# Optimization experiments

Hardware: AMD Instinct MI355X
Metric: run time of the kernel (lower is better)

Reference implementation:

```python
import jax, jax.numpy as jnp
import numpy as np

B = 4096
IN = 1723 * 6          # 10338
H = 1024
OUT = 24 * 3 * 3 + 10 + 3  # 229
EPS = 1e-5


def _bn(x, g, b):
    # BatchNorm1d training-mode forward: biased batch statistics
    mu = jnp.mean(x, axis=0)
    var = jnp.var(x, axis=0)
    return g * (x - mu) * jax.lax.rsqrt(var + EPS) + b


def _resblock(h, wa, ba, ga, bea, wb, bb, gb, beb):
    t = jax.nn.relu(_bn(h @ wa + ba, ga, bea))
    t = _bn(t @ wb + bb, gb, beb)
    return jax.nn.relu(h + t)


def setup_inputs() -> dict:
    key = jax.random.key(0)
    ks = jax.random.split(key, 16)
    s = 0.02
    inp = {"x": jax.random.normal(ks[0], (B, IN), dtype=jnp.float32)}
    # FCBlock(IN -> H): Linear + BN + ReLU
    inp["w1"] = jax.random.normal(ks[1], (IN, H), dtype=jnp.float32) * s
    inp["b1"] = jnp.zeros((H,), jnp.float32)
    inp["g1"] = jnp.ones((H,), jnp.float32)
    inp["be1"] = jnp.zeros((H,), jnp.float32)
    # two FCResBlocks (H -> H)
    for i, kk in zip((2, 3), (ks[2:4], ks[4:6])):
        inp[f"w{i}a"] = jax.random.normal(kk[0], (H, H), dtype=jnp.float32) * s
        inp[f"b{i}a"] = jnp.zeros((H,), jnp.float32)
        inp[f"g{i}a"] = jnp.ones((H,), jnp.float32)
        inp[f"be{i}a"] = jnp.zeros((H,), jnp.float32)
        inp[f"w{i}b"] = jax.random.normal(kk[1], (H, H), dtype=jnp.float32) * s
        inp[f"b{i}b"] = jnp.zeros((H,), jnp.float32)
        inp[f"g{i}b"] = jnp.ones((H,), jnp.float32)
        inp[f"be{i}b"] = jnp.zeros((H,), jnp.float32)
    # final Linear (H -> OUT)
    inp["w4"] = jax.random.normal(ks[6], (H, OUT), dtype=jnp.float32) * s
    inp["b4"] = jnp.zeros((OUT,), jnp.float32)
    return inp


def reference(x, w1, b1, g1, be1,
              w2a, b2a, g2a, be2a, w2b, b2b, g2b, be2b,
              w3a, b3a, g3a, be3a, w3b, b3b, g3b, be3b,
              w4, b4):
    batch = x.shape[0]
    h = jax.nn.relu(_bn(x @ w1 + b1, g1, be1))
    h = _resblock(h, w2a, b2a, g2a, be2a, w2b, b2b, g2b, be2b)
    h = _resblock(h, w3a, b3a, g3a, be3a, w3b, b3b, g3b, be3b)
    out = h @ w4 + b4                              # (B, 229)

    rotmat = out[:, :216].reshape(-1, 3, 3)        # (B*24, 3, 3)
    betas = out[:, 216:226]                        # (B, 10)
    camera = out[:, 226:]                          # (B, 3)

    # batched 3x3 SVD orthogonalization (replaces per-sample Python loop)
    U, S, Vh = jnp.linalg.svd(rotmat, full_matrices=False)
    R = U @ Vh
    # det computed under no_grad in original -> stop_gradient
    det = jax.lax.stop_gradient(jnp.linalg.det(R))[:, None, None]
    R = (R * det).reshape(batch, 24, 3, 3)
    return (R, betas, camera)
```

## Files before the change

### kernel.cpp

```cpp
#include <hip/hip_runtime.h>
#include <math.h>


typedef _Float16 half8 __attribute__((ext_vector_type(8)));
typedef _Float16 half4_t __attribute__((ext_vector_type(4)));
typedef float floatx4 __attribute__((ext_vector_type(4)));

#define LO_SCALE 4096.0f
#define LO_INV (1.0f / 4096.0f)
#define IN_C 10338
#define INP_C 10368

__device__ __forceinline__ void gld16(const _Float16* g, _Float16* l) {
  __builtin_amdgcn_global_load_lds(
      (const __attribute__((address_space(1))) void*)g,
      (__attribute__((address_space(3))) void*)l, 16, 0, 0);
}

template <int TAG, bool STATS>
__global__ __launch_bounds__(256, 2)
void gemm_sk(const _Float16* __restrict__ Ah, const _Float16* __restrict__ Al,
             const _Float16* __restrict__ Bh, const _Float16* __restrict__ Bl,
             float* __restrict__ Cp, int Kld, int Ncols, int Ks,
             size_t partStride, const float* __restrict__ bias,
             float* __restrict__ psum, float* __restrict__ psq) {
  __shared__ _Float16 sAh[2][4096], sAl[2][4096];
  __shared__ _Float16 sBh[2][4096], sBl[2][4096];
  const int tid = threadIdx.x;
  const int wv = tid >> 6, ln = tid & 63;
  const int ln15 = ln & 15, q = ln >> 4;
  const int wr = wv >> 1, wc = wv & 1;
  const int bm0 = blockIdx.x * 128, bn0 = blockIdx.y * 128;
  const int k0 = blockIdx.z * Ks;
  Cp += (size_t)blockIdx.z * partStride;

  const int srow = ln >> 2;
  const int swzw = (ln & 3) ^ (srow & 3) ^ ((srow >> 2) & 3);
  const int ch0 = wv * 2, ch1 = wv * 2 + 1;
  const size_t offA0 = (size_t)(bm0 + ch0 * 16 + srow) * Kld + k0 + swzw * 8;
  const size_t offA1 = (size_t)(bm0 + ch1 * 16 + srow) * Kld + k0 + swzw * 8;
  const size_t offB0 = (size_t)(bn0 + ch0 * 16 + srow) * Kld + k0 + swzw * 8;
  const size_t offB1 = (size_t)(bn0 + ch1 * 16 + srow) * Kld + k0 + swzw * 8;

  const int swzr = (q ^ (ln15 & 3) ^ ((ln15 >> 2) & 3)) * 8;
  const int aoff = (wr * 64 + ln15) * 32 + swzr;
  const int boff = (wc * 64 + ln15) * 32 + swzr;

  floatx4 acc[4][4];
  floatx4 acc2[4][4];
#pragma unroll
  for (int i = 0; i < 4; ++i)
#pragma unroll
    for (int j = 0; j < 4; ++j) {
      acc[i][j] = (floatx4){0.f, 0.f, 0.f, 0.f};
      acc2[i][j] = (floatx4){0.f, 0.f, 0.f, 0.f};
    }

  auto stage = [&](int kt, int buf) {
    gld16(Ah + offA0 + kt, &sAh[buf][ch0 * 512]);
    gld16(Ah + offA1 + kt, &sAh[buf][ch1 * 512]);
    gld16(Al + offA0 + kt, &sAl[buf][ch0 * 512]);
    gld16(Al + offA1 + kt, &sAl[buf][ch1 * 512]);
    gld16(Bh + offB0 + kt, &sBh[buf][ch0 * 512]);
    gld16(Bh + offB1 + kt, &sBh[buf][ch1 * 512]);
    gld16(Bl + offB0 + kt, &sBl[buf][ch0 * 512]);
    gld16(Bl + offB1 + kt, &sBl[buf][ch1 * 512]);
  };

  stage(0, 0);
  int cur = 0;
  for (int kt = 0; kt < Ks; kt += 32) {
    __syncthreads();
    if (kt + 32 < Ks) stage(kt + 32, cur ^ 1);

    const _Float16* pAh = &sAh[cur][aoff];
    const _Float16* pAl = &sAl[cur][aoff];
    const _Float16* pBh = &sBh[cur][boff];
    const _Float16* pBl = &sBl[cur][boff];
    half8 bh[4], bl[4];
#pragma unroll
    for (int ni = 0; ni < 4; ++ni) {
      bh[ni] = *(const half8*)(pBh + ni * 512);
      bl[ni] = *(const half8*)(pBl + ni * 512);
    }
#pragma unroll
    for (int mh = 0; mh < 2; ++mh) {
      half8 ah[2], al[2];
#pragma unroll
      for (int i = 0; i < 2; ++i) {
        ah[i] = *(const half8*)(pAh + (mh * 2 + i) * 512);
        al[i] = *(const half8*)(pAl + (mh * 2 + i) * 512);
      }
#pragma unroll
      for (int i = 0; i < 2; ++i) {
        const int mi = mh * 2 + i;
#pragma unroll
        for (int ni = 0; ni < 4; ++ni) {
          acc[mi][ni] = __builtin_amdgcn_mfma_f32_16x16x32_f16(
              ah[i], bh[ni], acc[mi][ni], 0, 0, 0);
          acc2[mi][ni] = __builtin_amdgcn_mfma_f32_16x16x32_f16(
              ah[i], bl[ni], acc2[mi][ni], 0, 0, 0);
          acc2[mi][ni] = __builtin_amdgcn_mfma_f32_16x16x32_f16(
              al[i], bh[ni], acc2[mi][ni], 0, 0, 0);
        }
      }
    }
    cur ^= 1;
  }

  float bs[4];
  float sacc[4] = {0.f, 0.f, 0.f, 0.f};
  float qacc[4] = {0.f, 0.f, 0.f, 0.f};
  if constexpr (STATS) {
#pragma unroll
    for (int ni = 0; ni < 4; ++ni)
      bs[ni] = bias[bn0 + wc * 64 + ni * 16 + ln15];
  }
#pragma unroll
  for (int mi = 0; mi < 4; ++mi)
#pragma unroll
    for (int ni = 0; ni < 4; ++ni) {
      const int col = bn0 + wc * 64 + ni * 16 + ln15;
      const int rbase = bm0 + wr * 64 + mi * 16 + q * 4;
#pragma unroll
      for (int r = 0; r < 4; ++r) {
        float v = acc[mi][ni][r] + acc2[mi][ni][r] * LO_INV;
        if constexpr (STATS) {
          v += bs[ni];
          sacc[ni] += v;
          qacc[ni] += v * v;
        }
        Cp[(size_t)(rbase + r) * Ncols + col] = v;
      }
    }
  if constexpr (STATS) {
    __syncthreads();
    float* sS = (float*)&sAh[0][0];
    float* sQ = (float*)&sAl[0][0];
    const int contrib = wr * 4 + q;
#pragma unroll
    for (int ni = 0; ni < 4; ++ni) {
      const int colt = wc * 64 + ni * 16 + ln15;
      sS[contrib * 128 + colt] = sacc[ni];
      sQ[contrib * 128 + colt] = qacc[ni];
    }
    __syncthreads();
    if (tid < 128) {
      float S = 0.f, Q = 0.f;
#pragma unroll
      for (int c = 0; c < 8; ++c) {
        S += sS[c * 128 + tid];
        Q += sQ[c * 128 + tid];
      }
      psum[(size_t)blockIdx.x * 1024 + bn0 + tid] = S;
      psq[(size_t)blockIdx.x * 1024 + bn0 + tid] = Q;
    }
  }
}

__global__ __launch_bounds__(256, 2)
void gemm_mid(const _Float16* __restrict__ Ah, const _Float16* __restrict__ Al,
              const _Float16* __restrict__ Bh, const _Float16* __restrict__ Bl,
              float* __restrict__ Y, int Kld, int Ncols, int Ks,
              const float* __restrict__ bias, float* __restrict__ psum,
              float* __restrict__ psq) {
  __shared__ _Float16 sAh[2][4096], sAl[2][4096];
  __shared__ _Float16 sBh[2][2048], sBl[2][2048];
  const int tid = threadIdx.x;
  const int wv = tid >> 6, ln = tid & 63;
  const int ln15 = ln & 15, q = ln >> 4;
  const int wr = wv >> 1, wc = wv & 1;
  const int bm0 = blockIdx.x * 128, bn0 = blockIdx.y * 64;

  const int srow = ln >> 2;
  const int swzw = (ln & 3) ^ (srow & 3) ^ ((srow >> 2) & 3);
  const int ch0 = wv * 2, ch1 = wv * 2 + 1;
  const size_t offA0 = (size_t)(bm0 + ch0 * 16 + srow) * Kld + swzw * 8;
  const size_t offA1 = (size_t)(bm0 + ch1 * 16 + srow) * Kld + swzw * 8;
  const size_t offB = (size_t)(bn0 + wv * 16 + srow) * Kld + swzw * 8;

  const int swzr = (q ^ (ln15 & 3) ^ ((ln15 >> 2) & 3)) * 8;
  const int aoff = (wr * 64 + ln15) * 32 + swzr;
  const int boff = (wc * 32 + ln15) * 32 + swzr;

  floatx4 acc[4][2], acc2[4][2];
#pragma unroll
  for (int i = 0; i < 4; ++i)
#pragma unroll
    for (int j = 0; j < 2; ++j) {
      acc[i][j] = (floatx4){0.f, 0.f, 0.f, 0.f};
      acc2[i][j] = (floatx4){0.f, 0.f, 0.f, 0.f};
    }

  auto stage = [&](int kt, int buf) {
    gld16(Ah + offA0 + kt, &sAh[buf][ch0 * 512]);
    gld16(Ah + offA1 + kt, &sAh[buf][ch1 * 512]);
    gld16(Al + offA0 + kt, &sAl[buf][ch0 * 512]);
    gld16(Al + offA1 + kt, &sAl[buf][ch1 * 512]);
    gld16(Bh + offB + kt, &sBh[buf][wv * 512]);
    gld16(Bl + offB + kt, &sBl[buf][wv * 512]);
  };

  stage(0, 0);
  int cur = 0;
  for (int kt = 0; kt < Ks; kt += 32) {
    __syncthreads();
    if (kt + 32 < Ks) stage(kt + 32, cur ^ 1);

    const _Float16* pAh = &sAh[cur][aoff];
    const _Float16* pAl = &sAl[cur][aoff];
    const _Float16* pBh = &sBh[cur][boff];
    const _Float16* pBl = &sBl[cur][boff];
    half8 bh[2], bl[2];
#pragma unroll
    for (int ni = 0; ni < 2; ++ni) {
      bh[ni] = *(const half8*)(pBh + ni * 512);
      bl[ni] = *(const half8*)(pBl + ni * 512);
    }
#pragma unroll
    for (int mh = 0; mh < 2; ++mh) {
      half8 ah[2], al[2];
#pragma unroll
      for (int i = 0; i < 2; ++i) {
        ah[i] = *(const half8*)(pAh + (mh * 2 + i) * 512);
        al[i] = *(const half8*)(pAl + (mh * 2 + i) * 512);
      }
#pragma unroll
      for (int i = 0; i < 2; ++i) {
        const int mi = mh * 2 + i;
#pragma unroll
        for (int ni = 0; ni < 2; ++ni) {
          acc[mi][ni] = __builtin_amdgcn_mfma_f32_16x16x32_f16(
              ah[i], bh[ni], acc[mi][ni], 0, 0, 0);
          acc2[mi][ni] = __builtin_amdgcn_mfma_f32_16x16x32_f16(
              ah[i], bl[ni], acc2[mi][ni], 0, 0, 0);
          acc2[mi][ni] = __builtin_amdgcn_mfma_f32_16x16x32_f16(
              al[i], bh[ni], acc2[mi][ni], 0, 0, 0);
        }
      }
    }
    cur ^= 1;
  }

  float bs[2];
  float sacc[2] = {0.f, 0.f};
  float qacc[2] = {0.f, 0.f};
#pragma unroll
  for (int ni = 0; ni < 2; ++ni)
    bs[ni] = bias[bn0 + wc * 32 + ni * 16 + ln15];
#pragma unroll
  for (int mi = 0; mi < 4; ++mi)
#pragma unroll
    for (int ni = 0; ni < 2; ++ni) {
      const int col = bn0 + wc * 32 + ni * 16 + ln15;
      const int rbase = bm0 + wr * 64 + mi * 16 + q * 4;
#pragma unroll
      for (int r = 0; r < 4; ++r) {
        float v = acc[mi][ni][r] + acc2[mi][ni][r] * LO_INV + bs[ni];
        sacc[ni] += v;
        qacc[ni] += v * v;
        Y[(size_t)(rbase + r) * Ncols + col] = v;
      }
    }
  __syncthreads();
  float* sS = (float*)&sAh[0][0];
  float* sQ = (float*)&sAl[0][0];
  const int contrib = wr * 4 + q;
#pragma unroll
  for (int ni = 0; ni < 2; ++ni) {
    const int colt = wc * 32 + ni * 16 + ln15;
    sS[contrib * 64 + colt] = sacc[ni];
    sQ[contrib * 64 + colt] = qacc[ni];
  }
  __syncthreads();
  if (tid < 64) {
    float S = 0.f, Q = 0.f;
#pragma unroll
    for (int c = 0; c < 8; ++c) {
      S += sS[c * 64 + tid];
      Q += sQ[c * 64 + tid];
    }
    psum[(size_t)blockIdx.x * 1024 + bn0 + tid] = S;
    psq[(size_t)blockIdx.x * 1024 + bn0 + tid] = Q;
  }
}

struct TJob {
  const float* src;
  _Float16* th;
  _Float16* tl;
  int K, N, Kpad, tK, start;
};
struct CJobs {
  TJob j[6];
  const float* x;
  _Float16* xh;
  _Float16* xl;
  int splitStart;
};

__global__ __launch_bounds__(256)
void convert_all(CJobs J) {
  const int b = blockIdx.x;
  const int tid = threadIdx.x;
  if (b >= J.splitStart) {
    int di = (b - J.splitStart) * 256 + tid;
    int base = di * 8;
    int row = base / INP_C;
    int col0 = base - row * INP_C;
    const float* src = J.x + (size_t)row * IN_C + col0;
    float v[8];
#pragma unroll
    for (int j = 0; j < 8; ++j) v[j] = (col0 + j < IN_C) ? src[j] : 0.f;
    half8 h, l;
#pragma unroll
    for (int j = 0; j < 8; ++j) {
      _Float16 hh = (_Float16)v[j];
      h[j] = hh;
      l[j] = (_Float16)((v[j] - (float)hh) * LO_SCALE);
    }
    *(half8*)(J.xh + base) = h;
    *(half8*)(J.xl + base) = l;
    return;
  }
  int ji = 0;
#pragma unroll
  for (int i = 1; i < 6; ++i)
    if (b >= J.j[i].start) ji = i;
  const TJob job = J.j[ji];
  const int t = b - job.start;
  const int kk0 = (t % job.tK) * 32;
  const int nn0 = (t / job.tK) * 32;

  __shared__ float ts[32][33];
  const int tx = tid & 31, ty = tid >> 5;
#pragma unroll
  for (int r = 0; r < 4; ++r) {
    int kk = kk0 + ty + r * 8;
    int nn = nn0 + tx;
    ts[ty + r * 8][tx] =
        (kk < job.K && nn < job.N) ? job.src[(size_t)kk * job.N + nn] : 0.f;
  }
  __syncthreads();
  const int tw = tid & 7, rw = tid >> 3;
  const int nn = nn0 + rw, kk = kk0 + tw * 4;
  half4_t h, l;
#pragma unroll
  for (int i2 = 0; i2 < 4; ++i2) {
    float v = ts[tw * 4 + i2][rw];
    _Float16 hh = (_Float16)v;
    h[i2] = hh;
    l[i2] = (_Float16)((v - (float)hh) * LO_SCALE);
  }
  size_t o = (size_t)nn * job.Kpad + kk;
  *(half4_t*)(job.th + o) = h;
  *(half4_t*)(job.tl + o) = l;
}

__global__ __launch_bounds__(256)
void reduce_bias_stats_v(const float* Cp, const float* __restrict__ bias,
                         float* Y, float* __restrict__ psum,
                         float* __restrict__ psq, int S, size_t stride,
                         int rowsPer) {
  const int N = 1024;
  const int t = threadIdx.x;
  const int cg = t & 15, rl = t >> 4;
  const int col4 = blockIdx.x * 64 + cg * 4;
  const int r0 = blockIdx.y * rowsPer;
  const floatx4 bs = *(const floatx4*)(bias + col4);
  floatx4 s = {0.f, 0.f, 0.f, 0.f}, qq = {0.f, 0.f, 0.f, 0.f};
  for (int r = r0 + rl; r < r0 + rowsPer; r += 16) {
    size_t i = (size_t)r * N + col4;
    floatx4 v = bs;
    for (int k = 0; k < S; ++k) v += *(const floatx4*)(Cp + k * stride + i);
    *(floatx4*)(Y + i) = v;
    s += v;
    qq += v * v;
  }
  __shared__ floatx4 ls[16][16], lq[16][16];
  ls[rl][cg] = s;
  lq[rl][cg] = qq;
  __syncthreads();
  if (t < 16) {
    floatx4 S4 = {0.f, 0.f, 0.f, 0.f}, Q4 = {0.f, 0.f, 0.f, 0.f};
#pragma unroll
    for (int r = 0; r < 16; ++r) {
      S4 += ls[r][t];
      Q4 += lq[r][t];
    }
    size_t o = (size_t)blockIdx.y * N + blockIdx.x * 64 + t * 4;
    *(floatx4*)(psum + o) = S4;
    *(floatx4*)(psq + o) = Q4;
  }
}

__global__ __launch_bounds__(256)
void bn_apply_v(const float* __restrict__ Y, const float* __restrict__ psum,
                const float* __restrict__ psq, const float* __restrict__ g,
                const float* __restrict__ be, const float* __restrict__ res,
                float* __restrict__ outf, _Float16* __restrict__ oh,
                _Float16* __restrict__ ol, int RB, float invM) {
  const int N = 1024;
  const int t = threadIdx.x;
  const int cg = t & 63, rl = t >> 6;
  const int col4 = blockIdx.x * 256 + cg * 4;
  __shared__ floatx4 lA[64], lB[64];
  if (t < 64) {
    int c4 = blockIdx.x * 256 + t * 4;
    floatx4 s = {0.f, 0.f, 0.f, 0.f}, qq = {0.f, 0.f, 0.f, 0.f};
    for (int rb = 0; rb < RB; ++rb) {
      s += *(const floatx4*)(psum + (size_t)rb * N + c4);
      qq += *(const floatx4*)(psq + (size_t)rb * N + c4);
    }
    floatx4 m = s * invM;
    floatx4 var = qq * invM - m * m;
    floatx4 rstd;
#pragma unroll
    for (int i = 0; i < 4; ++i) rstd[i] = rsqrtf(var[i] + 1e-5f);
    floatx4 a = (*(const floatx4*)(g + c4)) * rstd;
    lA[t] = a;
    lB[t] = (*(const floatx4*)(be + c4)) - m * a;
  }
  __syncthreads();
  const floatx4 a = lA[cg], b2 = lB[cg];
#pragma unroll
  for (int rr = 0; rr < 2; ++rr) {
    const int r = blockIdx.y * 8 + rl + rr * 4;
    const size_t i = (size_t)r * N + col4;
    floatx4 v = (*(const floatx4*)(Y + i)) * a + b2;
    if (res) v += *(const floatx4*)(res + i);
#pragma unroll
    for (int ii = 0; ii < 4; ++ii) v[ii] = fmaxf(v[ii], 0.f);
    if (outf) *(floatx4*)(outf + i) = v;
    half4_t h, l;
#pragma unroll
    for (int ii = 0; ii < 4; ++ii) {
      _Float16 hh = (_Float16)v[ii];
      h[ii] = hh;
      l[ii] = (_Float16)((v[ii] - (float)hh) * LO_SCALE);
    }
    *(half4_t*)(oh + i) = h;
    *(half4_t*)(ol + i) = l;
  }
}

__device__ __forceinline__ void cofactor3(const float X[9], float C[9]) {
  C[0] = X[4] * X[8] - X[5] * X[7];
  C[1] = X[5] * X[6] - X[3] * X[8];
  C[2] = X[3] * X[7] - X[4] * X[6];
  C[3] = X[2] * X[7] - X[1] * X[8];
  C[4] = X[0] * X[8] - X[2] * X[6];
  C[5] = X[1] * X[6] - X[0] * X[7];
  C[6] = X[1] * X[5] - X[2] * X[4];
  C[7] = X[2] * X[3] - X[0] * X[5];
  C[8] = X[0] * X[4] - X[1] * X[3];
}

__global__ __launch_bounds__(256)
void polar_tail(const float* __restrict__ Cp, const float* __restrict__ bias,
                float* __restrict__ out, int Bt, int nmat, int S,
                size_t stride) {
  const int ldy = 256;
  int idx = blockIdx.x * blockDim.x + threadIdx.x;
  if (idx < nmat) {
    int s = idx / 24, j = idx % 24;
    const size_t base = (size_t)s * ldy + j * 9;
    float A[9], X[9];
#pragma unroll
    for (int k = 0; k < 9; ++k) {
      float v = bias[j * 9 + k];
      for (int z = 0; z < S; ++z) v += Cp[z * stride + base + k];
      A[k] = v;
      X[k] = v;
    }
    double detA = (double)A[0] * ((double)A[4] * A[8] - (double)A[5] * A[7]) -
                  (double)A[1] * ((double)A[3] * A[8] - (double)A[5] * A[6]) +
                  (double)A[2] * ((double)A[3] * A[7] - (double)A[4] * A[6]);
    float sgn = (detA < 0.0) ? -1.f : 1.f;
#pragma unroll 1
    for (int it = 0; it < 12; ++it) {
      float C[9];
      cofactor3(X, C);
      float det = X[0] * C[0] + X[1] * C[1] + X[2] * C[2];
      float ad = fmaxf(fabsf(det), 1e-30f);
      float idet = (det < 0.f ? -1.f : 1.f) / ad;
      float n1 = 0.f, n2 = 0.f;
#pragma unroll
      for (int k = 0; k < 9; ++k) {
        n1 += X[k] * X[k];
        n2 += C[k] * C[k];
      }
      n1 = fmaxf(n1, 1e-30f);
      float zeta = sqrtf(sqrtf(n2 * idet * idet / n1));
      zeta = fminf(fmaxf(zeta, 1e-4f), 1e4f);
      float iz = 0.5f / zeta;
      float hz = 0.5f * zeta;
#pragma unroll
      for (int k = 0; k < 9; ++k) X[k] = hz * X[k] + iz * idet * C[k];
    }
    float* o = out + (size_t)idx * 9;
#pragma unroll
    for (int k = 0; k < 9; ++k) o[k] = X[k] * sgn;
  } else {
    int i = idx - nmat;
    int nb = Bt * 10;
    int nc = Bt * 3;
    int s, k, c;
    if (i < nb) {
      s = i / 10;
      k = i;
      c = 216 + (i % 10);
    } else if (i < nb + nc) {
      int t2 = i - nb;
      s = t2 / 3;
      k = i;
      c = 226 + (t2 % 3);
    } else {
      return;
    }
    float v = bias[c];
    size_t base = (size_t)s * ldy + c;
    for (int z = 0; z < S; ++z) v += Cp[z * stride + base];
    out[(size_t)Bt * 216 + k] = v;
  }
}

extern "C" void kernel_launch(void* const* d_in, const int* in_sizes, int n_in,
                              void* d_out, int out_size, void* d_ws,
                              size_t ws_size, hipStream_t stream) {
  const float* x = (const float*)d_in[0];
  const float* w1 = (const float*)d_in[1];
  const float* b1 = (const float*)d_in[2];
  const float* g1 = (const float*)d_in[3];
  const float* be1 = (const float*)d_in[4];
  const float* w2a = (const float*)d_in[5];
  const float* b2a = (const float*)d_in[6];
  const float* g2a = (const float*)d_in[7];
  const float* be2a = (const float*)d_in[8];
  const float* w2b = (const float*)d_in[9];
  const float* b2b = (const float*)d_in[10];
  const float* g2b = (const float*)d_in[11];
  const float* be2b = (const float*)d_in[12];
  const float* w3a = (const float*)d_in[13];
  const float* b3a = (const float*)d_in[14];
  const float* g3a = (const float*)d_in[15];
  const float* be3a = (const float*)d_in[16];
  const float* w3b = (const float*)d_in[17];
  const float* b3b = (const float*)d_in[18];
  const float* g3b = (const float*)d_in[19];
  const float* be3b = (const float*)d_in[20];
  const float* w4 = (const float*)d_in[21];
  const float* b4 = (const float*)d_in[22];
  float* out = (float*)d_out;

  const int B = 4096, IN = 10338, INP = 10368, H = 1024;
  const int OUTN = 229, OUTP = 256;
  const int RB = 32;
  const int S_L1 = 2, S_HEAD = 8;

  char* p = (char*)d_ws;
  auto alloc = [&](size_t bytes) -> void* {
    void* r = (void*)p;
    p += (bytes + 255) & ~(size_t)255;
    return r;
  };
  float* Cpart = (float*)alloc((size_t)4 * B * H * 4);
  float* Y = Cpart + 2 * (size_t)B * H;
  float* Hf = Cpart + 3 * (size_t)B * H;
  _Float16* xh = (_Float16*)alloc((size_t)B * INP * 2);
  _Float16* xl = (_Float16*)alloc((size_t)B * INP * 2);
  _Float16* w1h = (_Float16*)alloc((size_t)H * INP * 2);
  _Float16* w1l = (_Float16*)alloc((size_t)H * INP * 2);
  _Float16 *wmh[4], *wml[4];
  for (int i = 0; i < 4; ++i) {
    wmh[i] = (_Float16*)alloc((size_t)H * H * 2);
    wml[i] = (_Float16*)alloc((size_t)H * H * 2);
  }
  _Float16* w4h = (_Float16*)alloc((size_t)OUTP * H * 2);
  _Float16* w4l = (_Float16*)alloc((size_t)OUTP * H * 2);
  _Float16* hh = (_Float16*)alloc((size_t)B * H * 2);
  _Float16* hl = (_Float16*)alloc((size_t)B * H * 2);
  float* psum = (float*)alloc((size_t)RB * H * 4);
  float* psq = (float*)alloc((size_t)RB * H * 4);

  {
    CJobs J;
    const float* wsrc[6] = {w1, w2a, w2b, w3a, w3b, w4};
    _Float16* th[6] = {w1h, wmh[0], wmh[1], wmh[2], wmh[3], w4h};
    _Float16* tl[6] = {w1l, wml[0], wml[1], wml[2], wml[3], w4l};
    int Ks[6] = {IN, H, H, H, H, H};
    int Ns[6] = {H, H, H, H, H, OUTN};
    int Kpads[6] = {INP, H, H, H, H, H};
    int Npads[6] = {H, H, H, H, H, OUTP};
    int start = 0;
    for (int i = 0; i < 6; ++i) {
      J.j[i].src = wsrc[i];
      J.j[i].th = th[i];
      J.j[i].tl = tl[i];
      J.j[i].K = Ks[i];
      J.j[i].N = Ns[i];
      J.j[i].Kpad = Kpads[i];
      J.j[i].tK = Kpads[i] / 32;
      J.j[i].start = start;
      start += (Kpads[i] / 32) * (Npads[i] / 32);
    }
    J.x = x;
    J.xh = xh;
    J.xl = xl;
    J.splitStart = start;
    int total = start + (B * INP / 8 + 255) / 256;
    convert_all<<<dim3(total), 256, 0, stream>>>(J);
  }

  auto bnapply = [&](const float* g, const float* be, const float* res,
                     float* outf) {
    bn_apply_v<<<dim3(H / 256, B / 8), 256, 0, stream>>>(
        Y, psum, psq, g, be, res, outf, hh, hl, RB, 1.f / B);
  };
  auto midgemm = [&](const _Float16* Bh, const _Float16* Bl,
                     const float* bias) {
    gemm_mid<<<dim3(B / 128, H / 64, 1), 256, 0, stream>>>(
        hh, hl, Bh, Bl, Y, H, H, H, bias, psum, psq);
  };

  gemm_sk<0, false><<<dim3(B / 128, H / 128, S_L1), 256, 0, stream>>>(
      xh, xl, w1h, w1l, Cpart, INP, H, INP / S_L1, (size_t)B * H, nullptr,
      nullptr, nullptr);
  reduce_bias_stats_v<<<dim3(16, RB), 256, 0, stream>>>(
      Cpart, b1, Y, psum, psq, S_L1, (size_t)B * H, B / RB);
  bnapply(g1, be1, nullptr, Hf);
  midgemm(wmh[0], wml[0], b2a);
  bnapply(g2a, be2a, nullptr, nullptr);
  midgemm(wmh[1], wml[1], b2b);
  bnapply(g2b, be2b, Hf, Hf);
  midgemm(wmh[2], wml[2], b3a);
  bnapply(g3a, be3a, nullptr, nullptr);
  midgemm(wmh[3], wml[3], b3b);
  bnapply(g3b, be3b, Hf, Hf);
  gemm_sk<2, false><<<dim3(B / 128, OUTP / 128, S_HEAD), 256, 0, stream>>>(
      hh, hl, w4h, w4l, Cpart, H, OUTP, H / S_HEAD, (size_t)B * OUTP, nullptr,
      nullptr, nullptr);

  int nmat = B * 24;
  int ntot = nmat + B * 13;
  polar_tail<<<dim3((ntot + 255) / 256), 256, 0, stream>>>(
      Cpart, b4, out, B, nmat, S_HEAD, (size_t)B * OUTP);
}
```

Before: 887.6 us.

## Add narrower 128x64 tile kernel for first layer GEMM with three-way split-K

```diff
diff --git a/kernel.cpp b/kernel.cpp
--- a/kernel.cpp
+++ b/kernel.cpp
@@ -15,6 +15,104 @@
   __builtin_amdgcn_global_load_lds(
       (const __attribute__((address_space(1))) void*)g,
       (__attribute__((address_space(3))) void*)l, 16, 0, 0);
+}
+
+__global__ __launch_bounds__(256, 3)
+void gemm_l1(const _Float16* __restrict__ Ah, const _Float16* __restrict__ Al,
+             const _Float16* __restrict__ Bh, const _Float16* __restrict__ Bl,
+             float* __restrict__ Cp, int Kld, int Ncols, int Ks,
+             size_t partStride) {
+  __shared__ _Float16 sAh[2][4096], sAl[2][4096];
+  __shared__ _Float16 sBh[2][2048], sBl[2][2048];
+  const int tid = threadIdx.x;
+  const int wv = tid >> 6, ln = tid & 63;
+  const int ln15 = ln & 15, q = ln >> 4;
+  const int wr = wv >> 1, wc = wv & 1;
+  const int bm0 = blockIdx.x * 128, bn0 = blockIdx.y * 64;
+  const int k0 = blockIdx.z * Ks;
+  Cp += (size_t)blockIdx.z * partStride;
+
+  const int srow = ln >> 2;
+  const int swzw = (ln & 3) ^ (srow & 3) ^ ((srow >> 2) & 3);
+  const int ch0 = wv * 2, ch1 = wv * 2 + 1;
+  const size_t offA0 = (size_t)(bm0 + ch0 * 16 + srow) * Kld + k0 + swzw * 8;
+  const size_t offA1 = (size_t)(bm0 + ch1 * 16 + srow) * Kld + k0 + swzw * 8;
+  const size_t offB = (size_t)(bn0 + wv * 16 + srow) * Kld + k0 + swzw * 8;
+
+  const int swzr = (q ^ (ln15 & 3) ^ ((ln15 >> 2) & 3)) * 8;
+  const int aoff = (wr * 64 + ln15) * 32 + swzr;
+  const int boff = (wc * 32 + ln15) * 32 + swzr;
+
+  floatx4 acc[4][2], acc2[4][2];
+#pragma unroll
+  for (int i = 0; i < 4; ++i)
+#pragma unroll
+    for (int j = 0; j < 2; ++j) {
+      acc[i][j] = (floatx4){0.f, 0.f, 0.f, 0.f};
+      acc2[i][j] = (floatx4){0.f, 0.f, 0.f, 0.f};
+    }
+
+  auto stage = [&](int kt, int buf) {
+    gld16(Ah + offA0 + kt, &sAh[buf][ch0 * 512]);
+    gld16(Ah + offA1 + kt, &sAh[buf][ch1 * 512]);
+    gld16(Al + offA0 + kt, &sAl[buf][ch0 * 512]);
+    gld16(Al + offA1 + kt, &sAl[buf][ch1 * 512]);
+    gld16(Bh + offB + kt, &sBh[buf][wv * 512]);
+    gld16(Bl + offB + kt, &sBl[buf][wv * 512]);
+  };
+
+  stage(0, 0);
+  int cur = 0;
+  for (int kt = 0; kt < Ks; kt += 32) {
+    __syncthreads();
+    if (kt + 32 < Ks) stage(kt + 32, cur ^ 1);
+
+    const _Float16* pAh = &sAh[cur][aoff];
+    const _Float16* pAl = &sAl[cur][aoff];
+    const _Float16* pBh = &sBh[cur][boff];
+    const _Float16* pBl = &sBl[cur][boff];
+    half8 bh[2], bl[2];
+#pragma unroll
+    for (int ni = 0; ni < 2; ++ni) {
+      bh[ni] = *(const half8*)(pBh + ni * 512);
+      bl[ni] = *(const half8*)(pBl + ni * 512);
+    }
+#pragma unroll
+    for (int mh = 0; mh < 2; ++mh) {
+      half8 ah[2], al[2];
+#pragma unroll
+      for (int i = 0; i < 2; ++i) {
+        ah[i] = *(const half8*)(pAh + (mh * 2 + i) * 512);
+        al[i] = *(const half8*)(pAl + (mh * 2 + i) * 512);
+      }
+#pragma unroll
+      for (int i = 0; i < 2; ++i) {
+        const int mi = mh * 2 + i;
+#pragma unroll
+        for (int ni = 0; ni < 2; ++ni) {
+          acc[mi][ni] = __builtin_amdgcn_mfma_f32_16x16x32_f16(
+              ah[i], bh[ni], acc[mi][ni], 0, 0, 0);
+          acc2[mi][ni] = __builtin_amdgcn_mfma_f32_16x16x32_f16(
+              ah[i], bl[ni], acc2[mi][ni], 0, 0, 0);
+          acc2[mi][ni] = __builtin_amdgcn_mfma_f32_16x16x32_f16(
+              al[i], bh[ni], acc2[mi][ni], 0, 0, 0);
+        }
+      }
+    }
+    cur ^= 1;
+  }
+
+#pragma unroll
+  for (int mi = 0; mi < 4; ++mi)
+#pragma unroll
+    for (int ni = 0; ni < 2; ++ni) {
+      const int col = bn0 + wc * 32 + ni * 16 + ln15;
+      const int rbase = bm0 + wr * 64 + mi * 16 + q * 4;
+#pragma unroll
+      for (int r = 0; r < 4; ++r)
+        Cp[(size_t)(rbase + r) * Ncols + col] =
+            acc[mi][ni][r] + acc2[mi][ni][r] * LO_INV;
+    }
 }
 
 template <int TAG, bool STATS>
@@ -108,14 +206,6 @@
     cur ^= 1;
   }
 
-  float bs[4];
-  float sacc[4] = {0.f, 0.f, 0.f, 0.f};
-  float qacc[4] = {0.f, 0.f, 0.f, 0.f};
-  if constexpr (STATS) {
-#pragma unroll
-    for (int ni = 0; ni < 4; ++ni)
-      bs[ni] = bias[bn0 + wc * 64 + ni * 16 + ln15];
-  }
 #pragma unroll
   for (int mi = 0; mi < 4; ++mi)
 #pragma unroll
@@ -123,39 +213,10 @@
       const int col = bn0 + wc * 64 + ni * 16 + ln15;
       const int rbase = bm0 + wr * 64 + mi * 16 + q * 4;
 #pragma unroll
-      for (int r = 0; r < 4; ++r) {
-        float v = acc[mi][ni][r] + acc2[mi][ni][r] * LO_INV;
-        if constexpr (STATS) {
-          v += bs[ni];
-          sacc[ni] += v;
-          qacc[ni] += v * v;
-        }
-        Cp[(size_t)(rbase + r) * Ncols + col] = v;
-      }
-    }
-  if constexpr (STATS) {
-    __syncthreads();
-    float* sS = (float*)&sAh[0][0];
-    float* sQ = (float*)&sAl[0][0];
-    const int contrib = wr * 4 + q;
-#pragma unroll
-    for (int ni = 0; ni < 4; ++ni) {
-      const int colt = wc * 64 + ni * 16 + ln15;
-      sS[contrib * 128 + colt] = sacc[ni];
-      sQ[contrib * 128 + colt] = qacc[ni];
-    }
-    __syncthreads();
-    if (tid < 128) {
-      float S = 0.f, Q = 0.f;
-#pragma unroll
-      for (int c = 0; c < 8; ++c) {
-        S += sS[c * 128 + tid];
-        Q += sQ[c * 128 + tid];
-      }
-      psum[(size_t)blockIdx.x * 1024 + bn0 + tid] = S;
-      psq[(size_t)blockIdx.x * 1024 + bn0 + tid] = Q;
-    }
-  }
+      for (int r = 0; r < 4; ++r)
+        Cp[(size_t)(rbase + r) * Ncols + col] =
+            acc[mi][ni][r] + acc2[mi][ni][r] * LO_INV;
+    }
 }
 
 __global__ __launch_bounds__(256, 2)
@@ -556,7 +617,7 @@
   const int B = 4096, IN = 10338, INP = 10368, H = 1024;
   const int OUTN = 229, OUTP = 256;
   const int RB = 32;
-  const int S_L1 = 2, S_HEAD = 8;
+  const int S_L1 = 3, S_HEAD = 8;
 
   char* p = (char*)d_ws;
   auto alloc = [&](size_t bytes) -> void* {
@@ -564,9 +625,9 @@
     p += (bytes + 255) & ~(size_t)255;
     return r;
   };
-  float* Cpart = (float*)alloc((size_t)4 * B * H * 4);
-  float* Y = Cpart + 2 * (size_t)B * H;
-  float* Hf = Cpart + 3 * (size_t)B * H;
+  float* Cpart = (float*)alloc((size_t)5 * B * H * 4);
+  float* Y = Cpart + 3 * (size_t)B * H;
+  float* Hf = Cpart + 4 * (size_t)B * H;
   _Float16* xh = (_Float16*)alloc((size_t)B * INP * 2);
   _Float16* xl = (_Float16*)alloc((size_t)B * INP * 2);
   _Float16* w1h = (_Float16*)alloc((size_t)H * INP * 2);
@@ -623,9 +684,8 @@
         hh, hl, Bh, Bl, Y, H, H, H, bias, psum, psq);
   };
 
-  gemm_sk<0, false><<<dim3(B / 128, H / 128, S_L1), 256, 0, stream>>>(
-      xh, xl, w1h, w1l, Cpart, INP, H, INP / S_L1, (size_t)B * H, nullptr,
-      nullptr, nullptr);
+  gemm_l1<<<dim3(B / 128, H / 64, S_L1), 256, 0, stream>>>(
+      xh, xl, w1h, w1l, Cpart, INP, H, INP / S_L1, (size_t)B * H);
   reduce_bias_stats_v<<<dim3(16, RB), 256, 0, stream>>>(
       Cpart, b1, Y, psum, psq, S_L1, (size_t)B * H, B / RB);
   bnapply(g1, be1, nullptr, Hf);
```

Result: slower. 955.0 us (+7.6%).
